# Optimization experiments

Hardware: AMD Instinct MI355X
Metric: run time of the kernel (lower is better)

## Reference

```python
import jax, jax.numpy as jnp
import numpy as np

N_NODES = 100000
NEG_SLOPE = 0.2  # PyG GATConv default


def gat_conv(x, src, dst, W, a_src, a_dst, n_nodes):
    """One PyG-style GATConv (with self-loops already appended to src/dst).
    x: [N, Fin], W: [Fin, H*C], a_src/a_dst: [H, C]. Returns [N, H, C]."""
    H, C = a_src.shape
    h = (x @ W).reshape(-1, H, C)                      # [N, H, C]
    s_src = jnp.einsum('nhc,hc->nh', h, a_src)         # [N, H]
    s_dst = jnp.einsum('nhc,hc->nh', h, a_dst)         # [N, H]
    e = jax.nn.leaky_relu(s_src[src] + s_dst[dst], NEG_SLOPE)  # [E, H]
    # segment softmax over incoming edges of each destination node
    e_max = jax.ops.segment_max(e, dst, num_segments=n_nodes)  # [N, H]
    e_exp = jnp.exp(e - e_max[dst])
    denom = jax.ops.segment_sum(e_exp, dst, num_segments=n_nodes)
    alpha = e_exp / (denom[dst] + 1e-16)               # [E, H]
    msg = h[src] * alpha[:, :, None]                   # [E, H, C]
    return jax.ops.segment_sum(msg, dst, num_segments=n_nodes)  # [N, H, C]


def setup_inputs() -> dict:
    key = jax.random.key(0)
    ks = jax.random.split(key, 10)
    in_dim, hidden, heads, out_dim = 128, 32, 4, 32
    N, E = N_NODES, 1600000
    x = jax.random.normal(ks[0], (N, in_dim), dtype=jnp.float32)
    edge_index = jax.random.randint(ks[1], (2, E), 0, N, dtype=jnp.int64)
    s = 0.1
    return {
        'x': x,
        'edge_index': edge_index,
        'W1': s * jax.random.normal(ks[2], (in_dim, heads * hidden), dtype=jnp.float32),
        'a_src1': s * jax.random.normal(ks[3], (heads, hidden), dtype=jnp.float32),
        'a_dst1': s * jax.random.normal(ks[4], (heads, hidden), dtype=jnp.float32),
        'b1': jnp.zeros((heads * hidden,), dtype=jnp.float32),
        'W2': s * jax.random.normal(ks[5], (heads * hidden, out_dim), dtype=jnp.float32),
        'a_src2': s * jax.random.normal(ks[6], (1, out_dim), dtype=jnp.float32),
        'a_dst2': s * jax.random.normal(ks[7], (1, out_dim), dtype=jnp.float32),
        'b2': jnp.zeros((out_dim,), dtype=jnp.float32),
    }


def reference(x, edge_index, W1, a_src1, a_dst1, b1, W2, a_src2, a_dst2, b2):
    N = x.shape[0]
    loops = jnp.arange(N, dtype=edge_index.dtype)
    src = jnp.concatenate([edge_index[0], loops])  # PyG adds self-loops
    dst = jnp.concatenate([edge_index[1], loops])
    h1 = gat_conv(x, src, dst, W1, a_src1, a_dst1, N)      # [N, H, C]
    h1 = jax.nn.elu(h1.reshape(N, -1) + b1)                # concat heads + bias, elu
    h2 = gat_conv(h1, src, dst, W2, a_src2, a_dst2, N)     # [N, 1, out]
    return h2.mean(axis=1) + b2                            # concat=False -> mean over heads
```

## Files before the change

### kernel.cpp

```cpp
#include <hip/hip_runtime.h>
#include <hip/hip_bf16.h>

#define NEG 0.2f
#define BK_SHIFT 9
#define BK_CAP 9216

typedef short short8 __attribute__((ext_vector_type(8)));
typedef float f32x4 __attribute__((ext_vector_type(4)));

__device__ __forceinline__ float lrelu(float x){ return x > 0.f ? x : NEG * x; }
__device__ __forceinline__ float elu_f(float x){ return x > 0.f ? x : expm1f(x); }
__device__ __forceinline__ unsigned short f2bf(float f){
  unsigned int u = __float_as_uint(f);
  unsigned int r = u + 0x7fffu + ((u >> 16) & 1u);
  return (unsigned short)(r >> 16);
}
__device__ __forceinline__ float bf2f(unsigned short u){
  return __uint_as_float(((unsigned int)u) << 16);
}
__device__ __forceinline__ float2 bfu2(unsigned int v){
  float2 r;
  r.x = __uint_as_float(v << 16);
  r.y = __uint_as_float(v & 0xffff0000u);
  return r;
}

#define EB_SRC_MASK 0x7fffffu

__global__ __launch_bounds__(512) void k_binA_packW(
    const int* __restrict__ src, const int* __restrict__ dst, int E,
    int* __restrict__ gcursor, unsigned int* __restrict__ ebuf,
    const float* __restrict__ W, unsigned short* __restrict__ Wp, int nA){
  __shared__ int hist[256];
  __shared__ int base[256];
  int t = threadIdx.x;
  int bid = blockIdx.x;
  if (bid >= nA){
    int idx = (bid - nA) * 512 + t;
    int n = idx >> 7, k = idx & 127;
    Wp[n * 128 + k] = f2bf(W[(size_t)k * 128 + n]);
    return;
  }
  if (t < 256) hist[t] = 0;
  __syncthreads();
  int e0 = bid * 4096;
  for (int j = 0; j < 8; j++){
    int e = e0 + j * 512 + t;
    if (e < E) atomicAdd(&hist[dst[e] >> BK_SHIFT], 1);
  }
  __syncthreads();
  if (t < 256){
    int cnt = hist[t];
    if (cnt > 0) base[t] = atomicAdd(&gcursor[t], cnt);
    hist[t] = 0;
  }
  __syncthreads();
  for (int j = 0; j < 8; j++){
    int e = e0 + j * 512 + t;
    if (e < E){
      int d = dst[e]; int b = d >> BK_SHIFT;
      int loc = atomicAdd(&hist[b], 1);
      unsigned int dloc = (unsigned int)(d & ((1 << BK_SHIFT) - 1));
      ebuf[(size_t)b * BK_CAP + base[b] + loc] = (unsigned int)src[e] | (dloc << 23);
    }
  }
}

__global__ __launch_bounds__(256, 3) void k_csrC_gemm1(
    const unsigned int* __restrict__ ebuf, const int* __restrict__ gcount,
    int* __restrict__ rowp, int* __restrict__ csr, int N, int NBK, int total,
    const float* __restrict__ x, const unsigned short* __restrict__ Wp,
    const float* __restrict__ a_src, const float* __restrict__ a_dst,
    unsigned short* __restrict__ h_bf, float* __restrict__ ss, float* __restrict__ sd){
  __shared__ __align__(16) unsigned short Wt[128 * 136];
  __shared__ __align__(16) unsigned short Xb[64 * 136];
  int t = threadIdx.x;

  if (blockIdx.x < (unsigned)NBK){
    int* hist = (int*)Wt;
    int* psum = hist + 512;
    int* bsum = psum + 256;
    int b = blockIdx.x;
    int nbase = b << BK_SHIFT;
    int cnt = gcount[b];
    const unsigned int* eb = ebuf + (size_t)b * BK_CAP;
    hist[t] = 0; hist[t + 256] = 0;
    int bv = 0;
    {
      int nodes = 0;
      if (t < NBK){ int nb = N - (t << BK_SHIFT); nodes = nb > 512 ? 512 : nb; bv = gcount[t] + nodes; }
      bsum[t] = bv;
    }
    __syncthreads();
    for (int off = 1; off < 256; off <<= 1){
      int xv = (t >= off) ? bsum[t - off] : 0;
      __syncthreads();
      bsum[t] += xv;
      __syncthreads();
    }
    for (int i = t; i < cnt; i += 256)
      atomicAdd(&hist[eb[i] >> 23], 1);
    __syncthreads();
    int v0 = hist[2 * t], v1 = hist[2 * t + 1];
    int ps = v0 + v1;
    psum[t] = ps;
    __syncthreads();
    for (int off = 1; off < 256; off <<= 1){
      int xv = (t >= off) ? psum[t - off] : 0;
      __syncthreads();
      psum[t] += xv;
      __syncthreads();
    }
    {
      int eo = psum[t] - ps;
      int bb = (b == 0) ? 0 : bsum[b - 1];
      int n0 = 2 * t, n1 = 2 * t + 1;
      int r0 = bb + eo + n0;
      int r1 = bb + eo + v0 + n1;
      if (nbase + n0 < N) rowp[nbase + n0] = r0;
      if (nbase + n1 < N) rowp[nbase + n1] = r1;
      hist[n0] = r0; hist[n1] = r1;
    }
    if (b == 0 && t == 0) rowp[N] = total;
    __syncthreads();
    for (int i = t; i < cnt; i += 256){
      unsigned int e = eb[i];
      int pos = atomicAdd(&hist[e >> 23], 1);
      csr[pos] = (int)(e & EB_SRC_MASK);
    }
    __syncthreads();
    {
      int n0 = 2 * t, n1 = 2 * t + 1;
      if (nbase + n0 < N) csr[hist[n0]] = nbase + n0;
      if (nbase + n1 < N) csr[hist[n1]] = nbase + n1;
    }
    return;
  }

  int rb = (blockIdx.x - NBK) * 64;

  #pragma unroll
  for (int j = 0; j < 8; j++){
    int fi = j * 256 + t;
    int n = fi >> 4, ch = fi & 15;
    *(uint4*)&Wt[n * 136 + ch * 8] = *(const uint4*)&Wp[n * 128 + ch * 8];
  }
  #pragma unroll
  for (int j = 0; j < 8; j++){
    int fi = j * 256 + t;
    int row = fi >> 5, k4 = (fi & 31) * 4;
    int gr = rb + row;
    float4 v = make_float4(0.f, 0.f, 0.f, 0.f);
    if (gr < N) v = *(const float4*)&x[(size_t)gr * 128 + k4];
    uint2 pk;
    pk.x = ((unsigned)f2bf(v.y) << 16) | f2bf(v.x);
    pk.y = ((unsigned)f2bf(v.w) << 16) | f2bf(v.z);
    *(uint2*)&Xb[row * 136 + k4] = pk;
  }
  __syncthreads();

  int w = t >> 6, l = t & 63;
  int m = l & 15, quad = l >> 4;
  f32x4 acc[8];
  #pragma unroll
  for (int ct = 0; ct < 8; ct++) acc[ct] = (f32x4){0.f, 0.f, 0.f, 0.f};

  #pragma unroll
  for (int kc = 0; kc < 4; kc++){
    short8 a = *(const short8*)&Xb[(w * 16 + m) * 136 + kc * 32 + quad * 8];
    #pragma unroll
    for (int ct = 0; ct < 8; ct++){
      short8 bfr = *(const short8*)&Wt[(ct * 16 + m) * 136 + kc * 32 + quad * 8];
      acc[ct] = __builtin_amdgcn_mfma_f32_16x16x32_bf16(a, bfr, acc[ct], 0, 0, 0);
    }
  }

  float as[8], ad[8];
  #pragma unroll
  for (int ct = 0; ct < 8; ct++){ as[ct] = a_src[ct * 16 + m]; ad[ct] = a_dst[ct * 16 + m]; }

  #pragma unroll
  for (int reg = 0; reg < 4; reg++){
    int gr = rb + w * 16 + quad * 4 + reg;
    bool ok = gr < N;
    if (ok){
      #pragma unroll
      for (int ct = 0; ct < 8; ct++)
        h_bf[(size_t)gr * 128 + ct * 16 + m] = f2bf(acc[ct][reg]);
    }
    #pragma unroll
    for (int hh = 0; hh < 4; hh++){
      float pss = acc[2*hh][reg] * as[2*hh] + acc[2*hh+1][reg] * as[2*hh+1];
      float pd = acc[2*hh][reg] * ad[2*hh] + acc[2*hh+1][reg] * ad[2*hh+1];
      pss += __shfl_xor(pss, 1, 16); pss += __shfl_xor(pss, 2, 16);
      pss += __shfl_xor(pss, 4, 16); pss += __shfl_xor(pss, 8, 16);
      pd += __shfl_xor(pd, 1, 16); pd += __shfl_xor(pd, 2, 16);
      pd += __shfl_xor(pd, 4, 16); pd += __shfl_xor(pd, 8, 16);
      if (m == 0 && ok){ ss[(size_t)gr * 4 + hh] = pss; sd[(size_t)gr * 4 + hh] = pd; }
    }
  }
}

__global__ __launch_bounds__(256) void k_agg1(
    const int* __restrict__ row_ptr, const int* __restrict__ csr_src,
    const float* __restrict__ ss, const float* __restrict__ sdst,
    const unsigned short* __restrict__ hb,
    unsigned int* __restrict__ out1_bf, int N){
  int n = blockIdx.x * 4 + (threadIdx.x >> 6);
  if (n >= N) return;
  int l = threadIdx.x & 63;
  int q  = (l & 7) + ((l >> 5) << 3);
  int hh = (l >> 3) & 3;
  int slot = l >> 4;
  int c = l & 15;
  int hd = c >> 2;
  float sdw = sdst[(size_t)n * 4 + hh];
  int beg = row_ptr[n], end = row_ptr[n + 1];

  float acc[8] = {0.f,0.f,0.f,0.f,0.f,0.f,0.f,0.f};
  float swacc = 0.f;

  int e = beg;
  int remaining = end - beg;
  int qc = q < remaining ? q : 0;
  int sj = csr_src[e + qc];
  float sv = ss[(size_t)sj * 4 + hh];

  while (remaining > 0){
    int cur = remaining > 16 ? 16 : remaining;
    float wv = (q < cur) ? __expf(lrelu(sv + sdw)) : 0.f;
    swacc += wv;
    int sjc = sj;
    int rn = remaining - 16;
    if (rn > 0){
      int qn = q < rn ? q : 0;
      sj = csr_src[e + 16 + qn];
      sv = ss[(size_t)sj * 4 + hh];
    }
    #pragma unroll
    for (int p = 0; p < 4; p++){
      int base_p = ((p & 1) << 2) + ((p >> 1) << 3);
      if (base_p < cur){
        int sl = ((p & 1) << 2) + slot + ((p >> 1) << 5);
        int s  = __shfl(sjc, sl, 64);
        float w = __shfl(wv, sl + (hd << 3), 64);
        if (base_p + slot < cur){
          uint4 u = *(const uint4*)&hb[(size_t)s * 128 + (c << 3)];
          float2 f0 = bfu2(u.x), f1 = bfu2(u.y), f2 = bfu2(u.z), f3 = bfu2(u.w);
          acc[0] += w * f0.x; acc[1] += w * f0.y;
          acc[2] += w * f1.x; acc[3] += w * f1.y;
          acc[4] += w * f2.x; acc[5] += w * f2.y;
          acc[6] += w * f3.x; acc[7] += w * f3.y;
        }
      }
    }
    e += 16; remaining = rn;
  }

  #pragma unroll
  for (int i = 0; i < 8; i++){
    acc[i] += __shfl_xor(acc[i], 16, 64);
    acc[i] += __shfl_xor(acc[i], 32, 64);
  }
  swacc += __shfl_xor(swacc, 1, 64);
  swacc += __shfl_xor(swacc, 2, 64);
  swacc += __shfl_xor(swacc, 4, 64);
  swacc += __shfl_xor(swacc, 32, 64);
  float sw = __shfl(swacc, hd << 3, 64);
  float inv = 1.f / (sw + 1e-16f);
  if (slot == 0){
    unsigned int o0 = ((unsigned)f2bf(acc[1] * inv) << 16) | f2bf(acc[0] * inv);
    unsigned int o1 = ((unsigned)f2bf(acc[3] * inv) << 16) | f2bf(acc[2] * inv);
    unsigned int o2 = ((unsigned)f2bf(acc[5] * inv) << 16) | f2bf(acc[4] * inv);
    unsigned int o3 = ((unsigned)f2bf(acc[7] * inv) << 16) | f2bf(acc[6] * inv);
    uint4 o; o.x = o0; o.y = o1; o.z = o2; o.w = o3;
    *(uint4*)&out1_bf[(size_t)n * 64 + (c << 2)] = o;
  }
}

__global__ __launch_bounds__(256) void k_gemm2(
    const unsigned int* __restrict__ out1_bf, const float* __restrict__ b1,
    const float* __restrict__ W2,
    const float* __restrict__ a_src, const float* __restrict__ a_dst,
    unsigned short* __restrict__ h2_bf, float* __restrict__ s_src2, float* __restrict__ s_dst2, int N){
  __shared__ __align__(16) float Wl[128 * 32];
  __shared__ __align__(16) float Xl[64 * 132];
  int t = threadIdx.x;
  int rb = blockIdx.x * 64;

  const float4* Wg4 = (const float4*)W2;
  float4* Wl4 = (float4*)Wl;
  #pragma unroll
  for (int j = 0; j < 4; j++) Wl4[j * 256 + t] = Wg4[j * 256 + t];

  #pragma unroll
  for (int j = 0; j < 4; j++){
    int fi = j * 256 + t;
    int row = fi >> 4, q = fi & 15;
    int gr = rb + row;
    float v[8] = {0.f,0.f,0.f,0.f,0.f,0.f,0.f,0.f};
    if (gr < N){
      uint4 u = *(const uint4*)&out1_bf[(size_t)gr * 64 + q * 4];
      float4 bva = *(const float4*)&b1[q * 8];
      float4 bvb = *(const float4*)&b1[q * 8 + 4];
      v[0] = elu_f(bf2f((unsigned short)(u.x & 0xffff)) + bva.x);
      v[1] = elu_f(bf2f((unsigned short)(u.x >> 16))    + bva.y);
      v[2] = elu_f(bf2f((unsigned short)(u.y & 0xffff)) + bva.z);
      v[3] = elu_f(bf2f((unsigned short)(u.y >> 16))    + bva.w);
      v[4] = elu_f(bf2f((unsigned short)(u.z & 0xffff)) + bvb.x);
      v[5] = elu_f(bf2f((unsigned short)(u.z >> 16))    + bvb.y);
      v[6] = elu_f(bf2f((unsigned short)(u.w & 0xffff)) + bvb.z);
      v[7] = elu_f(bf2f((unsigned short)(u.w >> 16))    + bvb.w);
    }
    #pragma unroll
    for (int i = 0; i < 8; i++) Xl[row * 132 + q * 8 + i] = v[i];
  }
  __syncthreads();

  int cg = t & 7, rg = t >> 3;
  int c0 = cg * 4, r0 = rg * 2;
  float acc[2][4] = {};

  #pragma unroll 8
  for (int k = 0; k < 128; k++){
    float a0 = Xl[r0 * 132 + k];
    float a1 = Xl[(r0 + 1) * 132 + k];
    float4 b = *(float4*)&Wl[k * 32 + c0];
    acc[0][0] += a0 * b.x; acc[0][1] += a0 * b.y; acc[0][2] += a0 * b.z; acc[0][3] += a0 * b.w;
    acc[1][0] += a1 * b.x; acc[1][1] += a1 * b.y; acc[1][2] += a1 * b.z; acc[1][3] += a1 * b.w;
  }

  float as[4], ad[4];
  #pragma unroll
  for (int j = 0; j < 4; j++){ as[j] = a_src[c0 + j]; ad[j] = a_dst[c0 + j]; }
  #pragma unroll
  for (int i = 0; i < 2; i++){
    int row = rb + r0 + i;
    if (row < N){
      ushort4 o;
      o.x = f2bf(acc[i][0]); o.y = f2bf(acc[i][1]); o.z = f2bf(acc[i][2]); o.w = f2bf(acc[i][3]);
      *(ushort4*)&h2_bf[(size_t)row * 32 + c0] = o;
    }
    float ps = 0.f, pd = 0.f;
    #pragma unroll
    for (int j = 0; j < 4; j++){ ps += acc[i][j] * as[j]; pd += acc[i][j] * ad[j]; }
    ps += __shfl_xor(ps, 1, 8); ps += __shfl_xor(ps, 2, 8); ps += __shfl_xor(ps, 4, 8);
    pd += __shfl_xor(pd, 1, 8); pd += __shfl_xor(pd, 2, 8); pd += __shfl_xor(pd, 4, 8);
    if ((t & 7) == 0 && row < N){ s_src2[row] = ps; s_dst2[row] = pd; }
  }
}

__global__ __launch_bounds__(256) void k_agg2(
    const int* __restrict__ row_ptr, const int* __restrict__ csr_src,
    const float* __restrict__ ss2, const float* __restrict__ sd2,
    const unsigned short* __restrict__ h2bf, const float* __restrict__ b2,
    float* __restrict__ out, int N){
  int n = blockIdx.x * 4 + (threadIdx.x >> 6);
  if (n >= N) return;
  int l = threadIdx.x & 63;
  int q = l & 15;
  int slot = l >> 2;
  int ch4 = l & 3;
  float sdv = sd2[n];
  int beg = row_ptr[n], end = row_ptr[n + 1];

  float acc[8] = {0.f,0.f,0.f,0.f,0.f,0.f,0.f,0.f};
  float swacc = 0.f;

  int e = beg;
  int remaining = end - beg;
  int qc = q < remaining ? q : 0;
  int sj = csr_src[e + qc];
  float sv = ss2[sj];

  while (remaining > 0){
    int cur = remaining > 16 ? 16 : remaining;
    float wv = (q < cur) ? __expf(lrelu(sv + sdv)) : 0.f;
    swacc += wv;
    int sjc = sj; float wvc = wv;
    int rn = remaining - 16;
    if (rn > 0){
      int qn = q < rn ? q : 0;
      sj = csr_src[e + 16 + qn];
      sv = ss2[sj];
    }
    {
      int s  = __shfl(sjc, slot, 64);
      float w = __shfl(wvc, slot, 64);
      if (slot < cur){
        uint4 u = *(const uint4*)&h2bf[(size_t)s * 32 + (ch4 << 3)];
        float2 f0 = bfu2(u.x), f1 = bfu2(u.y), f2 = bfu2(u.z), f3 = bfu2(u.w);
        acc[0] += w * f0.x; acc[1] += w * f0.y;
        acc[2] += w * f1.x; acc[3] += w * f1.y;
        acc[4] += w * f2.x; acc[5] += w * f2.y;
        acc[6] += w * f3.x; acc[7] += w * f3.y;
      }
    }
    e += 16; remaining = rn;
  }

  #pragma unroll
  for (int i = 0; i < 8; i++){
    acc[i] += __shfl_xor(acc[i], 4, 64);
    acc[i] += __shfl_xor(acc[i], 8, 64);
    acc[i] += __shfl_xor(acc[i], 16, 64);
    acc[i] += __shfl_xor(acc[i], 32, 64);
  }
  swacc += __shfl_xor(swacc, 1, 64);
  swacc += __shfl_xor(swacc, 2, 64);
  swacc += __shfl_xor(swacc, 4, 64);
  swacc += __shfl_xor(swacc, 8, 64);
  float inv = 1.f / (swacc + 1e-16f);
  if (slot == 0){
    float4 bva = *(const float4*)&b2[(ch4 << 3)];
    float4 bvb = *(const float4*)&b2[(ch4 << 3) + 4];
    float4 oa, ob;
    oa.x = acc[0] * inv + bva.x; oa.y = acc[1] * inv + bva.y;
    oa.z = acc[2] * inv + bva.z; oa.w = acc[3] * inv + bva.w;
    ob.x = acc[4] * inv + bvb.x; ob.y = acc[5] * inv + bvb.y;
    ob.z = acc[6] * inv + bvb.z; ob.w = acc[7] * inv + bvb.w;
    *(float4*)&out[(size_t)n * 32 + (ch4 << 3)] = oa;
    *(float4*)&out[(size_t)n * 32 + (ch4 << 3) + 4] = ob;
  }
}

extern "C" void kernel_launch(void* const* d_in, const int* in_sizes, int n_in,
                              void* d_out, int out_size, void* d_ws, size_t ws_size,
                              hipStream_t stream) {
  const float* x      = (const float*)d_in[0];
  const int*   ei     = (const int*)  d_in[1];
  const float* W1     = (const float*)d_in[2];
  const float* a_src1 = (const float*)d_in[3];
  const float* a_dst1 = (const float*)d_in[4];
  const float* b1     = (const float*)d_in[5];
  const float* W2     = (const float*)d_in[6];
  const float* a_src2 = (const float*)d_in[7];
  const float* a_dst2 = (const float*)d_in[8];
  const float* b2     = (const float*)d_in[9];
  float* out = (float*)d_out;

  int N = in_sizes[0] / 128;
  int E = in_sizes[1] / 2;
  const int* srcp = ei;
  const int* dstp = ei + E;
  int total = E + N;
  int NBK = (N + 511) >> 9;

  char* p = (char*)d_ws;
  auto alloc = [&](size_t bytes) -> void* {
    void* r = (void*)p; p += (bytes + 255) & ~(size_t)255; return r;
  };
  unsigned short* h_bf    = (unsigned short*)alloc((size_t)N * 128 * 2);
  unsigned int*   out1_bf = (unsigned int*)alloc((size_t)N * 64 * 4);
  unsigned short* h2_bf   = (unsigned short*)alloc((size_t)N * 32 * 2);
  unsigned short* Wp      = (unsigned short*)alloc(128 * 128 * 2);
  float* ss1  = (float*)alloc((size_t)N * 4 * 4);
  float* sd1  = (float*)alloc((size_t)N * 4 * 4);
  float* ss2  = (float*)alloc((size_t)N * 4);
  float* sd2  = (float*)alloc((size_t)N * 4);
  int* rowp   = (int*)alloc((size_t)(N + 1) * 4);
  int* csr    = (int*)alloc((size_t)total * 4);
  int* gcur   = (int*)alloc(256 * 4);
  unsigned int* ebuf = (unsigned int*)out1_bf;
  (void)ws_size; (void)n_in; (void)out_size;

  int nA = (E + 4095) / 4096;
  int nG = (N + 63) / 64;

  hipMemsetAsync(gcur, 0, 256 * 4, stream);
  k_binA_packW<<<nA + 32, 512, 0, stream>>>(srcp, dstp, E, gcur, ebuf, W1, Wp, nA);
  k_csrC_gemm1<<<NBK + nG, 256, 0, stream>>>(ebuf, gcur, rowp, csr, N, NBK, total,
                                             x, Wp, a_src1, a_dst1, h_bf, ss1, sd1);
  k_agg1<<<(N + 3) / 4, 256, 0, stream>>>(rowp, csr, ss1, sd1, h_bf, out1_bf, N);
  k_gemm2<<<nG, 256, 0, stream>>>(out1_bf, b1, W2, a_src2, a_dst2, h2_bf, ss2, sd2, N);
  k_agg2<<<(N + 3) / 4, 256, 0, stream>>>(rowp, csr, ss2, sd2, h2_bf, b2, out, N);
}
```

Baseline: 309.1 us.

## Fuse layer-1 aggregation with bias, ELU and layer-2 projection

Merges the first-layer aggregation kernel with the second-layer GEMM. Each wavefront applies bias and ELU to its aggregated node row, multiplies it by a swizzled shared-memory copy of W2, and reduces across lanes to produce h2 and the layer-2 attention scores directly. This removes the out1 intermediate write and read and one kernel launch. In exchange, every 25k block reloads W2 into LDS, and the per-slot bounds guard on the gather is dropped, so out-of-range slots now read row 0 with zero weight.

```diff
diff --git a/kernel.cpp b/kernel.cpp
--- a/kernel.cpp
+++ b/kernel.cpp
@@ -201,14 +201,29 @@
   }
 }
 
-__global__ __launch_bounds__(256) void k_agg1(
+__global__ __launch_bounds__(256) void k_agg1g2(
     const int* __restrict__ row_ptr, const int* __restrict__ csr_src,
     const float* __restrict__ ss, const float* __restrict__ sdst,
     const unsigned short* __restrict__ hb,
-    unsigned int* __restrict__ out1_bf, int N){
-  int n = blockIdx.x * 4 + (threadIdx.x >> 6);
+    const float* __restrict__ b1, const float* __restrict__ W2,
+    const float* __restrict__ a_src2, const float* __restrict__ a_dst2,
+    unsigned short* __restrict__ h2_bf, float* __restrict__ ss2, float* __restrict__ sd2,
+    int N){
+  __shared__ __align__(16) float Wl2[128 * 32];
+  __shared__ float Bl[128];
+  int t = threadIdx.x;
+  #pragma unroll
+  for (int j = 0; j < 16; j++){
+    int idx = j * 256 + t;
+    int row = idx >> 5, col = idx & 31;
+    Wl2[row * 32 + (col ^ (((row >> 3) & 7) << 2))] = W2[idx];
+  }
+  if (t < 128) Bl[t] = b1[t];
+  __syncthreads();
+
+  int n = blockIdx.x * 4 + (t >> 6);
   if (n >= N) return;
-  int l = threadIdx.x & 63;
+  int l = t & 63;
   int q  = (l & 7) + ((l >> 5) << 3);
   int hh = (l >> 3) & 3;
   int slot = l >> 4;
@@ -244,14 +259,12 @@
         int sl = ((p & 1) << 2) + slot + ((p >> 1) << 5);
         int s  = __shfl(sjc, sl, 64);
         float w = __shfl(wv, sl + (hd << 3), 64);
-        if (base_p + slot < cur){
-          uint4 u = *(const uint4*)&hb[(size_t)s * 128 + (c << 3)];
-          float2 f0 = bfu2(u.x), f1 = bfu2(u.y), f2 = bfu2(u.z), f3 = bfu2(u.w);
-          acc[0] += w * f0.x; acc[1] += w * f0.y;
-          acc[2] += w * f1.x; acc[3] += w * f1.y;
-          acc[4] += w * f2.x; acc[5] += w * f2.y;
-          acc[6] += w * f3.x; acc[7] += w * f3.y;
-        }
+        uint4 u = *(const uint4*)&hb[(size_t)s * 128 + (c << 3)];
+        float2 f0 = bfu2(u.x), f1 = bfu2(u.y), f2 = bfu2(u.z), f3 = bfu2(u.w);
+        acc[0] += w * f0.x; acc[1] += w * f0.y;
+        acc[2] += w * f1.x; acc[3] += w * f1.y;
+        acc[4] += w * f2.x; acc[5] += w * f2.y;
+        acc[6] += w * f3.x; acc[7] += w * f3.y;
       }
     }
     e += 16; remaining = rn;
@@ -268,86 +281,48 @@
   swacc += __shfl_xor(swacc, 32, 64);
   float sw = __shfl(swacc, hd << 3, 64);
   float inv = 1.f / (sw + 1e-16f);
-  if (slot == 0){
-    unsigned int o0 = ((unsigned)f2bf(acc[1] * inv) << 16) | f2bf(acc[0] * inv);
-    unsigned int o1 = ((unsigned)f2bf(acc[3] * inv) << 16) | f2bf(acc[2] * inv);
-    unsigned int o2 = ((unsigned)f2bf(acc[5] * inv) << 16) | f2bf(acc[4] * inv);
-    unsigned int o3 = ((unsigned)f2bf(acc[7] * inv) << 16) | f2bf(acc[6] * inv);
-    uint4 o; o.x = o0; o.y = o1; o.z = o2; o.w = o3;
-    *(uint4*)&out1_bf[(size_t)n * 64 + (c << 2)] = o;
-  }
-}
-
-__global__ __launch_bounds__(256) void k_gemm2(
-    const unsigned int* __restrict__ out1_bf, const float* __restrict__ b1,
-    const float* __restrict__ W2,
-    const float* __restrict__ a_src, const float* __restrict__ a_dst,
-    unsigned short* __restrict__ h2_bf, float* __restrict__ s_src2, float* __restrict__ s_dst2, int N){
-  __shared__ __align__(16) float Wl[128 * 32];
-  __shared__ __align__(16) float Xl[64 * 132];
-  int t = threadIdx.x;
-  int rb = blockIdx.x * 64;
-
-  const float4* Wg4 = (const float4*)W2;
-  float4* Wl4 = (float4*)Wl;
-  #pragma unroll
-  for (int j = 0; j < 4; j++) Wl4[j * 256 + t] = Wg4[j * 256 + t];
-
-  #pragma unroll
-  for (int j = 0; j < 4; j++){
-    int fi = j * 256 + t;
-    int row = fi >> 4, q = fi & 15;
-    int gr = rb + row;
-    float v[8] = {0.f,0.f,0.f,0.f,0.f,0.f,0.f,0.f};
-    if (gr < N){
-      uint4 u = *(const uint4*)&out1_bf[(size_t)gr * 64 + q * 4];
-      float4 bva = *(const float4*)&b1[q * 8];
-      float4 bvb = *(const float4*)&b1[q * 8 + 4];
-      v[0] = elu_f(bf2f((unsigned short)(u.x & 0xffff)) + bva.x);
-      v[1] = elu_f(bf2f((unsigned short)(u.x >> 16))    + bva.y);
-      v[2] = elu_f(bf2f((unsigned short)(u.y & 0xffff)) + bva.z);
-      v[3] = elu_f(bf2f((unsigned short)(u.y >> 16))    + bva.w);
-      v[4] = elu_f(bf2f((unsigned short)(u.z & 0xffff)) + bvb.x);
-      v[5] = elu_f(bf2f((unsigned short)(u.z >> 16))    + bvb.y);
-      v[6] = elu_f(bf2f((unsigned short)(u.w & 0xffff)) + bvb.z);
-      v[7] = elu_f(bf2f((unsigned short)(u.w >> 16))    + bvb.w);
-    }
-    #pragma unroll
-    for (int i = 0; i < 8; i++) Xl[row * 132 + q * 8 + i] = v[i];
-  }
-  __syncthreads();
-
-  int cg = t & 7, rg = t >> 3;
-  int c0 = cg * 4, r0 = rg * 2;
-  float acc[2][4] = {};
-
-  #pragma unroll 8
-  for (int k = 0; k < 128; k++){
-    float a0 = Xl[r0 * 132 + k];
-    float a1 = Xl[(r0 + 1) * 132 + k];
-    float4 b = *(float4*)&Wl[k * 32 + c0];
-    acc[0][0] += a0 * b.x; acc[0][1] += a0 * b.y; acc[0][2] += a0 * b.z; acc[0][3] += a0 * b.w;
-    acc[1][0] += a1 * b.x; acc[1][1] += a1 * b.y; acc[1][2] += a1 * b.z; acc[1][3] += a1 * b.w;
-  }
-
-  float as[4], ad[4];
-  #pragma unroll
-  for (int j = 0; j < 4; j++){ as[j] = a_src[c0 + j]; ad[j] = a_dst[c0 + j]; }
-  #pragma unroll
-  for (int i = 0; i < 2; i++){
-    int row = rb + r0 + i;
-    if (row < N){
-      ushort4 o;
-      o.x = f2bf(acc[i][0]); o.y = f2bf(acc[i][1]); o.z = f2bf(acc[i][2]); o.w = f2bf(acc[i][3]);
-      *(ushort4*)&h2_bf[(size_t)row * 32 + c0] = o;
-    }
-    float ps = 0.f, pd = 0.f;
-    #pragma unroll
-    for (int j = 0; j < 4; j++){ ps += acc[i][j] * as[j]; pd += acc[i][j] * ad[j]; }
-    ps += __shfl_xor(ps, 1, 8); ps += __shfl_xor(ps, 2, 8); ps += __shfl_xor(ps, 4, 8);
-    pd += __shfl_xor(pd, 1, 8); pd += __shfl_xor(pd, 2, 8); pd += __shfl_xor(pd, 4, 8);
-    if ((t & 7) == 0 && row < N){ s_src2[row] = ps; s_dst2[row] = pd; }
-  }
+
+  float y[8];
+  #pragma unroll
+  for (int i = 0; i < 8; i++) y[i] = elu_f(acc[i] * inv + Bl[8 * c + i]);
+
+  int o = (c & 7) << 2;
+  float h2v[8] = {0.f,0.f,0.f,0.f,0.f,0.f,0.f,0.f};
+  #pragma unroll
+  for (int i = 0; i < 8; i++){
+    int rw = (8 * c + i) * 32;
+    float4 wa = *(const float4*)&Wl2[rw + ((8 * slot) ^ o)];
+    float4 wb = *(const float4*)&Wl2[rw + ((8 * slot + 4) ^ o)];
+    h2v[0] += y[i] * wa.x; h2v[1] += y[i] * wa.y;
+    h2v[2] += y[i] * wa.z; h2v[3] += y[i] * wa.w;
+    h2v[4] += y[i] * wb.x; h2v[5] += y[i] * wb.y;
+    h2v[6] += y[i] * wb.z; h2v[7] += y[i] * wb.w;
+  }
+  #pragma unroll
+  for (int i = 0; i < 8; i++){
+    h2v[i] += __shfl_xor(h2v[i], 1, 64);
+    h2v[i] += __shfl_xor(h2v[i], 2, 64);
+    h2v[i] += __shfl_xor(h2v[i], 4, 64);
+    h2v[i] += __shfl_xor(h2v[i], 8, 64);
+  }
+  float ps2 = 0.f, pd2 = 0.f;
+  #pragma unroll
+  for (int i = 0; i < 8; i++){
+    ps2 += h2v[i] * a_src2[8 * slot + i];
+    pd2 += h2v[i] * a_dst2[8 * slot + i];
+  }
+  ps2 += __shfl_xor(ps2, 16, 64); ps2 += __shfl_xor(ps2, 32, 64);
+  pd2 += __shfl_xor(pd2, 16, 64); pd2 += __shfl_xor(pd2, 32, 64);
+
+  if (c == 0){
+    unsigned int p0 = ((unsigned)f2bf(h2v[1]) << 16) | f2bf(h2v[0]);
+    unsigned int p1 = ((unsigned)f2bf(h2v[3]) << 16) | f2bf(h2v[2]);
+    unsigned int p2 = ((unsigned)f2bf(h2v[5]) << 16) | f2bf(h2v[4]);
+    unsigned int p3 = ((unsigned)f2bf(h2v[7]) << 16) | f2bf(h2v[6]);
+    uint4 ov; ov.x = p0; ov.y = p1; ov.z = p2; ov.w = p3;
+    *(uint4*)&h2_bf[(size_t)n * 32 + 8 * slot] = ov;
+  }
+  if (l == 0){ ss2[n] = ps2; sd2[n] = pd2; }
 }
 
 __global__ __launch_bounds__(256) void k_agg2(
@@ -451,7 +426,7 @@
     void* r = (void*)p; p += (bytes + 255) & ~(size_t)255; return r;
   };
   unsigned short* h_bf    = (unsigned short*)alloc((size_t)N * 128 * 2);
-  unsigned int*   out1_bf = (unsigned int*)alloc((size_t)N * 64 * 4);
+  unsigned int*   ebuf    = (unsigned int*)alloc((size_t)256 * BK_CAP * 4);
   unsigned short* h2_bf   = (unsigned short*)alloc((size_t)N * 32 * 2);
   unsigned short* Wp      = (unsigned short*)alloc(128 * 128 * 2);
   float* ss1  = (float*)alloc((size_t)N * 4 * 4);
@@ -461,7 +436,6 @@
   int* rowp   = (int*)alloc((size_t)(N + 1) * 4);
   int* csr    = (int*)alloc((size_t)total * 4);
   int* gcur   = (int*)alloc(256 * 4);
-  unsigned int* ebuf = (unsigned int*)out1_bf;
   (void)ws_size; (void)n_in; (void)out_size;
 
   int nA = (E + 4095) / 4096;
@@ -471,7 +445,7 @@
   k_binA_packW<<<nA + 32, 512, 0, stream>>>(srcp, dstp, E, gcur, ebuf, W1, Wp, nA);
   k_csrC_gemm1<<<NBK + nG, 256, 0, stream>>>(ebuf, gcur, rowp, csr, N, NBK, total,
                                              x, Wp, a_src1, a_dst1, h_bf, ss1, sd1);
-  k_agg1<<<(N + 3) / 4, 256, 0, stream>>>(rowp, csr, ss1, sd1, h_bf, out1_bf, N);
-  k_gemm2<<<nG, 256, 0, stream>>>(out1_bf, b1, W2, a_src2, a_dst2, h2_bf, ss2, sd2, N);
+  k_agg1g2<<<(N + 3) / 4, 256, 0, stream>>>(rowp, csr, ss1, sd1, h_bf,
+                                            b1, W2, a_src2, a_dst2, h2_bf, ss2, sd2, N);
   k_agg2<<<(N + 3) / 4, 256, 0, stream>>>(rowp, csr, ss2, sd2, h2_bf, b2, out, N);
 }
```

After: 325.2 us. 5.2% more time.

## Use bf16 MFMA for layer-2 GEMM and cache edge loads in binning

Applied to the files above, without the earlier changes.

The second-layer GEMM moves from scalar fp32 FMA to bf16 MFMA 16x16x32, and W2 is pre-packed into transposed bf16 inside the binning kernel. Activations are written to LDS as bf16 after ELU, and ELU now uses __expf instead of expm1f. The binning kernel keeps src/dst in registers so edges are not read twice. The agg1 inner gather drops its per-slot bounds check and relies on zeroed weights for the tail. This cuts GEMM ALU time and redundant global loads, at the cost of bf16 input precision, a less accurate ELU near zero, and extra loads in the tail.

```diff
diff --git a/kernel.cpp b/kernel.cpp
--- a/kernel.cpp
+++ b/kernel.cpp
@@ -9,7 +9,7 @@
 typedef float f32x4 __attribute__((ext_vector_type(4)));
 
 __device__ __forceinline__ float lrelu(float x){ return x > 0.f ? x : NEG * x; }
-__device__ __forceinline__ float elu_f(float x){ return x > 0.f ? x : expm1f(x); }
+__device__ __forceinline__ float elu_fast(float x){ return x > 0.f ? x : __expf(x) - 1.f; }
 __device__ __forceinline__ unsigned short f2bf(float f){
   unsigned int u = __float_as_uint(f);
   unsigned int r = u + 0x7fffu + ((u >> 16) & 1u);
@@ -30,23 +30,35 @@
 __global__ __launch_bounds__(512) void k_binA_packW(
     const int* __restrict__ src, const int* __restrict__ dst, int E,
     int* __restrict__ gcursor, unsigned int* __restrict__ ebuf,
-    const float* __restrict__ W, unsigned short* __restrict__ Wp, int nA){
+    const float* __restrict__ W, unsigned short* __restrict__ Wp,
+    const float* __restrict__ W2, unsigned short* __restrict__ Wp2, int nA){
   __shared__ int hist[256];
   __shared__ int base[256];
   int t = threadIdx.x;
   int bid = blockIdx.x;
   if (bid >= nA){
     int idx = (bid - nA) * 512 + t;
-    int n = idx >> 7, k = idx & 127;
-    Wp[n * 128 + k] = f2bf(W[(size_t)k * 128 + n]);
+    if (idx < 16384){
+      int n = idx >> 7, k = idx & 127;
+      Wp[n * 128 + k] = f2bf(W[(size_t)k * 128 + n]);
+    } else {
+      int i2 = idx - 16384;
+      int n = i2 >> 7, k = i2 & 127;
+      Wp2[n * 128 + k] = f2bf(W2[(size_t)k * 32 + n]);
+    }
     return;
   }
   if (t < 256) hist[t] = 0;
   __syncthreads();
   int e0 = bid * 4096;
+  int dsr[8], ssr[8];
+  #pragma unroll
   for (int j = 0; j < 8; j++){
     int e = e0 + j * 512 + t;
-    if (e < E) atomicAdd(&hist[dst[e] >> BK_SHIFT], 1);
+    if (e < E){
+      dsr[j] = dst[e]; ssr[j] = src[e];
+      atomicAdd(&hist[dsr[j] >> BK_SHIFT], 1);
+    } else dsr[j] = -1;
   }
   __syncthreads();
   if (t < 256){
@@ -55,13 +67,13 @@
     hist[t] = 0;
   }
   __syncthreads();
+  #pragma unroll
   for (int j = 0; j < 8; j++){
-    int e = e0 + j * 512 + t;
-    if (e < E){
-      int d = dst[e]; int b = d >> BK_SHIFT;
+    if (dsr[j] >= 0){
+      int d = dsr[j]; int b = d >> BK_SHIFT;
       int loc = atomicAdd(&hist[b], 1);
       unsigned int dloc = (unsigned int)(d & ((1 << BK_SHIFT) - 1));
-      ebuf[(size_t)b * BK_CAP + base[b] + loc] = (unsigned int)src[e] | (dloc << 23);
+      ebuf[(size_t)b * BK_CAP + base[b] + loc] = (unsigned int)ssr[j] | (dloc << 23);
     }
   }
 }
@@ -244,14 +256,12 @@
         int sl = ((p & 1) << 2) + slot + ((p >> 1) << 5);
         int s  = __shfl(sjc, sl, 64);
         float w = __shfl(wv, sl + (hd << 3), 64);
-        if (base_p + slot < cur){
-          uint4 u = *(const uint4*)&hb[(size_t)s * 128 + (c << 3)];
-          float2 f0 = bfu2(u.x), f1 = bfu2(u.y), f2 = bfu2(u.z), f3 = bfu2(u.w);
-          acc[0] += w * f0.x; acc[1] += w * f0.y;
-          acc[2] += w * f1.x; acc[3] += w * f1.y;
-          acc[4] += w * f2.x; acc[5] += w * f2.y;
-          acc[6] += w * f3.x; acc[7] += w * f3.y;
-        }
+        uint4 u = *(const uint4*)&hb[(size_t)s * 128 + (c << 3)];
+        float2 f0 = bfu2(u.x), f1 = bfu2(u.y), f2 = bfu2(u.z), f3 = bfu2(u.w);
+        acc[0] += w * f0.x; acc[1] += w * f0.y;
+        acc[2] += w * f1.x; acc[3] += w * f1.y;
+        acc[4] += w * f2.x; acc[5] += w * f2.y;
+        acc[6] += w * f3.x; acc[7] += w * f3.y;
       }
     }
     e += 16; remaining = rn;
@@ -278,75 +288,83 @@
   }
 }
 
-__global__ __launch_bounds__(256) void k_gemm2(
+__global__ __launch_bounds__(256) void k_gemm2m(
     const unsigned int* __restrict__ out1_bf, const float* __restrict__ b1,
-    const float* __restrict__ W2,
+    const unsigned short* __restrict__ Wp2,
     const float* __restrict__ a_src, const float* __restrict__ a_dst,
-    unsigned short* __restrict__ h2_bf, float* __restrict__ s_src2, float* __restrict__ s_dst2, int N){
-  __shared__ __align__(16) float Wl[128 * 32];
-  __shared__ __align__(16) float Xl[64 * 132];
+    unsigned short* __restrict__ h2_bf, float* __restrict__ ss2, float* __restrict__ sd2, int N){
+  __shared__ __align__(16) unsigned short Wt[32 * 136];
+  __shared__ __align__(16) unsigned short Xb[64 * 136];
   int t = threadIdx.x;
   int rb = blockIdx.x * 64;
 
-  const float4* Wg4 = (const float4*)W2;
-  float4* Wl4 = (float4*)Wl;
-  #pragma unroll
-  for (int j = 0; j < 4; j++) Wl4[j * 256 + t] = Wg4[j * 256 + t];
-
+  #pragma unroll
+  for (int j = 0; j < 2; j++){
+    int fi = j * 256 + t;
+    int n = fi >> 4, ch = fi & 15;
+    *(uint4*)&Wt[n * 136 + ch * 8] = *(const uint4*)&Wp2[n * 128 + ch * 8];
+  }
   #pragma unroll
   for (int j = 0; j < 4; j++){
     int fi = j * 256 + t;
     int row = fi >> 4, q = fi & 15;
     int gr = rb + row;
-    float v[8] = {0.f,0.f,0.f,0.f,0.f,0.f,0.f,0.f};
+    uint4 o = make_uint4(0u, 0u, 0u, 0u);
     if (gr < N){
       uint4 u = *(const uint4*)&out1_bf[(size_t)gr * 64 + q * 4];
       float4 bva = *(const float4*)&b1[q * 8];
       float4 bvb = *(const float4*)&b1[q * 8 + 4];
-      v[0] = elu_f(bf2f((unsigned short)(u.x & 0xffff)) + bva.x);
-      v[1] = elu_f(bf2f((unsigned short)(u.x >> 16))    + bva.y);
-      v[2] = elu_f(bf2f((unsigned short)(u.y & 0xffff)) + bva.z);
-      v[3] = elu_f(bf2f((unsigned short)(u.y >> 16))    + bva.w);
-      v[4] = elu_f(bf2f((unsigned short)(u.z & 0xffff)) + bvb.x);
-      v[5] = elu_f(bf2f((unsigned short)(u.z >> 16))    + bvb.y);
-      v[6] = elu_f(bf2f((unsigned short)(u.w & 0xffff)) + bvb.z);
-      v[7] = elu_f(bf2f((unsigned short)(u.w >> 16))    + bvb.w);
-    }
+      float v0 = elu_fast(bf2f((unsigned short)(u.x & 0xffff)) + bva.x);
+      float v1 = elu_fast(bf2f((unsigned short)(u.x >> 16))    + bva.y);
+      float v2 = elu_fast(bf2f((unsigned short)(u.y & 0xffff)) + bva.z);
+      float v3 = elu_fast(bf2f((unsigned short)(u.y >> 16))    + bva.w);
+      float v4 = elu_fast(bf2f((unsigned short)(u.z & 0xffff)) + bvb.x);
+      float v5 = elu_fast(bf2f((unsigned short)(u.z >> 16))    + bvb.y);
+      float v6 = elu_fast(bf2f((unsigned short)(u.w & 0xffff)) + bvb.z);
+      float v7 = elu_fast(bf2f((unsigned short)(u.w >> 16))    + bvb.w);
+      o.x = ((unsigned)f2bf(v1) << 16) | f2bf(v0);
+      o.y = ((unsigned)f2bf(v3) << 16) | f2bf(v2);
+      o.z = ((unsigned)f2bf(v5) << 16) | f2bf(v4);
+      o.w = ((unsigned)f2bf(v7) << 16) | f2bf(v6);
+    }
+    *(uint4*)&Xb[row * 136 + q * 8] = o;
+  }
+  __syncthreads();
+
+  int w = t >> 6, l = t & 63;
+  int m = l & 15, quad = l >> 4;
+  f32x4 acc[2];
+  acc[0] = (f32x4){0.f, 0.f, 0.f, 0.f};
+  acc[1] = (f32x4){0.f, 0.f, 0.f, 0.f};
+
+  #pragma unroll
+  for (int kc = 0; kc < 4; kc++){
+    short8 a = *(const short8*)&Xb[(w * 16 + m) * 136 + kc * 32 + quad * 8];
     #pragma unroll
-    for (int i = 0; i < 8; i++) Xl[row * 132 + q * 8 + i] = v[i];
-  }
-  __syncthreads();
-
-  int cg = t & 7, rg = t >> 3;
-  int c0 = cg * 4, r0 = rg * 2;
-  float acc[2][4] = {};
-
-  #pragma unroll 8
-  for (int k = 0; k < 128; k++){
-    float a0 = Xl[r0 * 132 + k];
-    float a1 = Xl[(r0 + 1) * 132 + k];
-    float4 b = *(float4*)&Wl[k * 32 + c0];
-    acc[0][0] += a0 * b.x; acc[0][1] += a0 * b.y; acc[0][2] += a0 * b.z; acc[0][3] += a0 * b.w;
-    acc[1][0] += a1 * b.x; acc[1][1] += a1 * b.y; acc[1][2] += a1 * b.z; acc[1][3] += a1 * b.w;
-  }
-
-  float as[4], ad[4];
-  #pragma unroll
-  for (int j = 0; j < 4; j++){ as[j] = a_src[c0 + j]; ad[j] = a_dst[c0 + j]; }
-  #pragma unroll
-  for (int i = 0; i < 2; i++){
-    int row = rb + r0 + i;
-    if (row < N){
-      ushort4 o;
-      o.x = f2bf(acc[i][0]); o.y = f2bf(acc[i][1]); o.z = f2bf(acc[i][2]); o.w = f2bf(acc[i][3]);
-      *(ushort4*)&h2_bf[(size_t)row * 32 + c0] = o;
-    }
-    float ps = 0.f, pd = 0.f;
-    #pragma unroll
-    for (int j = 0; j < 4; j++){ ps += acc[i][j] * as[j]; pd += acc[i][j] * ad[j]; }
-    ps += __shfl_xor(ps, 1, 8); ps += __shfl_xor(ps, 2, 8); ps += __shfl_xor(ps, 4, 8);
-    pd += __shfl_xor(pd, 1, 8); pd += __shfl_xor(pd, 2, 8); pd += __shfl_xor(pd, 4, 8);
-    if ((t & 7) == 0 && row < N){ s_src2[row] = ps; s_dst2[row] = pd; }
+    for (int ct = 0; ct < 2; ct++){
+      short8 bfr = *(const short8*)&Wt[(ct * 16 + m) * 136 + kc * 32 + quad * 8];
+      acc[ct] = __builtin_amdgcn_mfma_f32_16x16x32_bf16(a, bfr, acc[ct], 0, 0, 0);
+    }
+  }
+
+  float as0 = a_src[m], as1 = a_src[16 + m];
+  float ad0 = a_dst[m], ad1 = a_dst[16 + m];
+
+  #pragma unroll
+  for (int reg = 0; reg < 4; reg++){
+    int gr = rb + w * 16 + quad * 4 + reg;
+    bool ok = gr < N;
+    if (ok){
+      h2_bf[(size_t)gr * 32 + m]      = f2bf(acc[0][reg]);
+      h2_bf[(size_t)gr * 32 + 16 + m] = f2bf(acc[1][reg]);
+    }
+    float ps = acc[0][reg] * as0 + acc[1][reg] * as1;
+    float pd = acc[0][reg] * ad0 + acc[1][reg] * ad1;
+    ps += __shfl_xor(ps, 1, 16); ps += __shfl_xor(ps, 2, 16);
+    ps += __shfl_xor(ps, 4, 16); ps += __shfl_xor(ps, 8, 16);
+    pd += __shfl_xor(pd, 1, 16); pd += __shfl_xor(pd, 2, 16);
+    pd += __shfl_xor(pd, 4, 16); pd += __shfl_xor(pd, 8, 16);
+    if (m == 0 && ok){ ss2[gr] = ps; sd2[gr] = pd; }
   }
 }
 
@@ -454,6 +472,7 @@
   unsigned int*   out1_bf = (unsigned int*)alloc((size_t)N * 64 * 4);
   unsigned short* h2_bf   = (unsigned short*)alloc((size_t)N * 32 * 2);
   unsigned short* Wp      = (unsigned short*)alloc(128 * 128 * 2);
+  unsigned short* Wp2     = (unsigned short*)alloc(32 * 128 * 2);
   float* ss1  = (float*)alloc((size_t)N * 4 * 4);
   float* sd1  = (float*)alloc((size_t)N * 4 * 4);
   float* ss2  = (float*)alloc((size_t)N * 4);
@@ -468,10 +487,10 @@
   int nG = (N + 63) / 64;
 
   hipMemsetAsync(gcur, 0, 256 * 4, stream);
-  k_binA_packW<<<nA + 32, 512, 0, stream>>>(srcp, dstp, E, gcur, ebuf, W1, Wp, nA);
+  k_binA_packW<<<nA + 40, 512, 0, stream>>>(srcp, dstp, E, gcur, ebuf, W1, Wp, W2, Wp2, nA);
   k_csrC_gemm1<<<NBK + nG, 256, 0, stream>>>(ebuf, gcur, rowp, csr, N, NBK, total,
                                              x, Wp, a_src1, a_dst1, h_bf, ss1, sd1);
   k_agg1<<<(N + 3) / 4, 256, 0, stream>>>(rowp, csr, ss1, sd1, h_bf, out1_bf, N);
-  k_gemm2<<<nG, 256, 0, stream>>>(out1_bf, b1, W2, a_src2, a_dst2, h2_bf, ss2, sd2, N);
+  k_gemm2m<<<nG, 256, 0, stream>>>(out1_bf, b1, Wp2, a_src2, a_dst2, h2_bf, ss2, sd2, N);
   k_agg2<<<(N + 3) / 4, 256, 0, stream>>>(rowp, csr, ss2, sd2, h2_bf, b2, out, N);
 }
```

Result: faster. 292.2 us (-5.5%).
